# Kernel tuning notes

Hardware: AMD Instinct MI355X
Metric: run time of the kernel (lower is better)

## Reference

```python
import jax, jax.numpy as jnp
import numpy as np

N_RNA, N_PROT, D, C, E = 20000, 5000, 128, 4, 500000

def setup_inputs() -> dict:
    key = jax.random.key(0)
    k1, k2, k3, k4, k5, k6 = jax.random.split(key, 6)
    return {
        "RNA_inputs": jax.random.normal(k1, (N_RNA, D), dtype=jnp.float32),
        "protein_inputs": jax.random.normal(k2, (N_PROT, D), dtype=jnp.float32),
        "RNA_indices": jax.random.randint(k3, (E,), 0, N_RNA, dtype=jnp.int64),
        "protein_indices": jax.random.randint(k4, (E,), 0, N_PROT, dtype=jnp.int64),
        "w_relation": jax.random.normal(k5, (C, D), dtype=jnp.float32),
        "weight_classifier": jax.random.normal(k6, (C, C), dtype=jnp.float32),
    }

def reference(RNA_inputs, protein_inputs, RNA_indices, protein_indices, w_relation, weight_classifier):
    # Gather node features for each pair (dropout p=0.0 -> identity)
    r = RNA_inputs[RNA_indices]        # [E, D]
    p = protein_inputs[protein_indices]  # [E, D]
    # Per-class bilinear: basis[e, c] = sum_d r[e,d] * w_relation[c,d] * p[e,d]
    basis = jnp.einsum('ed,cd->ec', r * p, w_relation)  # [E, C]
    # Classifier matmul + ReLU activation
    return jax.nn.relu(basis @ weight_classifier)  # [E, C]
```

## Files before the change

kernel.cpp:

```cpp
#include <hip/hip_runtime.h>

#define DIM 128
#define NCLS 4

typedef _Float16 f16x4 __attribute__((ext_vector_type(4)));
typedef _Float16 f16x8 __attribute__((ext_vector_type(8)));

__global__ __launch_bounds__(256) void cvt_both_kernel(
    const float* __restrict__ s1, _Float16* __restrict__ d1, int n1,
    const float* __restrict__ s2, _Float16* __restrict__ d2, int n2)
{
    const int total = n1 + n2;
    int i = (blockIdx.x * blockDim.x + threadIdx.x) * 8;
    const int stride = gridDim.x * blockDim.x * 8;
    for (; i < total; i += stride) {
        const float* s; _Float16* d; int j;
        if (i < n1) { s = s1; d = d1; j = i; }
        else        { s = s2; d = d2; j = i - n1; }
        const float4 a = *(const float4*)(s + j);
        const float4 b = *(const float4*)(s + j + 4);
        f16x8 o;
        o[0] = (_Float16)a.x; o[1] = (_Float16)a.y;
        o[2] = (_Float16)a.z; o[3] = (_Float16)a.w;
        o[4] = (_Float16)b.x; o[5] = (_Float16)b.y;
        o[6] = (_Float16)b.z; o[7] = (_Float16)b.w;
        *(f16x8*)(d + j) = o;
    }
}

__device__ __forceinline__ float reduce4(float b0, float b1, float b2, float b3, int lane)
{
    const bool lo1 = (lane & 1) == 0;
    float k0 = lo1 ? b0 : b2, s0 = lo1 ? b2 : b0;
    float k1 = lo1 ? b1 : b3, s1 = lo1 ? b3 : b1;
    float v0 = k0 + __shfl_xor(s0, 1, 32);
    float v1 = k1 + __shfl_xor(s1, 1, 32);
    const bool lo2 = (lane & 2) == 0;
    float k = lo2 ? v0 : v1, s = lo2 ? v1 : v0;
    float v = k + __shfl_xor(s, 2, 32);
    v += __shfl_xor(v, 4, 32);
    v += __shfl_xor(v, 8, 32);
    v += __shfl_xor(v, 16, 32);
    return v;
}

__device__ __forceinline__ void dot_store(
    f16x4 r, f16x4 p, const float4& wf0, const float4& wf1,
    const float4& wf2, const float4& wf3, int lane, int cls,
    float* __restrict__ out, long e)
{
    const f16x4 q = r * p;
    const float qx = (float)q[0], qy = (float)q[1];
    const float qz = (float)q[2], qw = (float)q[3];
    float b0 = qx * wf0.x + qy * wf0.y + qz * wf0.z + qw * wf0.w;
    float b1 = qx * wf1.x + qy * wf1.y + qz * wf1.z + qw * wf1.w;
    float b2 = qx * wf2.x + qy * wf2.y + qz * wf2.z + qw * wf2.w;
    float b3 = qx * wf3.x + qy * wf3.y + qz * wf3.z + qw * wf3.w;
    const float v = reduce4(b0, b1, b2, b3, lane);
    if (lane < 4) out[e * NCLS + cls] = fmaxf(v, 0.0f);
}

__global__ __launch_bounds__(256, 5) void decoder_ilp8_kernel(
    const _Float16* __restrict__ rna,
    const _Float16* __restrict__ prot,
    const int*   __restrict__ ridx,
    const int*   __restrict__ pidx,
    const float* __restrict__ wrel,
    const float* __restrict__ wcls,
    float*       __restrict__ out,
    int nEdges)
{
    const int l32 = threadIdx.x & 31;
    const int hw  = (blockIdx.x * blockDim.x + threadIdx.x) >> 5;
    const int nhw = (gridDim.x * blockDim.x) >> 5;

    const float4 w0 = *(const float4*)(wrel + 0 * DIM + l32 * 4);
    const float4 w1 = *(const float4*)(wrel + 1 * DIM + l32 * 4);
    const float4 w2 = *(const float4*)(wrel + 2 * DIM + l32 * 4);
    const float4 w3 = *(const float4*)(wrel + 3 * DIM + l32 * 4);
    float wc[16];
#pragma unroll
    for (int i = 0; i < 16; ++i) wc[i] = wcls[i];
    float4 wf0, wf1, wf2, wf3;
    {
        float4* wfp[4] = {&wf0, &wf1, &wf2, &wf3};
#pragma unroll
        for (int j = 0; j < 4; ++j) {
            wfp[j]->x = wc[j] * w0.x + wc[4 + j] * w1.x + wc[8 + j] * w2.x + wc[12 + j] * w3.x;
            wfp[j]->y = wc[j] * w0.y + wc[4 + j] * w1.y + wc[8 + j] * w2.y + wc[12 + j] * w3.y;
            wfp[j]->z = wc[j] * w0.z + wc[4 + j] * w1.z + wc[8 + j] * w2.z + wc[12 + j] * w3.z;
            wfp[j]->w = wc[j] * w0.w + wc[4 + j] * w1.w + wc[8 + j] * w2.w + wc[12 + j] * w3.w;
        }
    }
    const int cls = ((l32 & 1) << 1) | ((l32 >> 1) & 1);

    const long step = (long)nhw * 8;
    long e0 = (long)hw * 8;
    if (e0 + 7 >= nEdges) return;

    int4 riA = *(const int4*)(ridx + e0);
    int4 piA = *(const int4*)(pidx + e0);
    int4 riB = *(const int4*)(ridx + e0 + 4);
    int4 piB = *(const int4*)(pidx + e0 + 4);

    for (;;) {
        const f16x4 rA0 = ((const f16x4*)(rna + (size_t)riA.x * DIM))[l32];
        const f16x4 rA1 = ((const f16x4*)(rna + (size_t)riA.y * DIM))[l32];
        const f16x4 rA2 = ((const f16x4*)(rna + (size_t)riA.z * DIM))[l32];
        const f16x4 rA3 = ((const f16x4*)(rna + (size_t)riA.w * DIM))[l32];
        const f16x4 pA0 = ((const f16x4*)(prot + (size_t)piA.x * DIM))[l32];
        const f16x4 pA1 = ((const f16x4*)(prot + (size_t)piA.y * DIM))[l32];
        const f16x4 pA2 = ((const f16x4*)(prot + (size_t)piA.z * DIM))[l32];
        const f16x4 pA3 = ((const f16x4*)(prot + (size_t)piA.w * DIM))[l32];
        const f16x4 rB0 = ((const f16x4*)(rna + (size_t)riB.x * DIM))[l32];
        const f16x4 rB1 = ((const f16x4*)(rna + (size_t)riB.y * DIM))[l32];
        const f16x4 rB2 = ((const f16x4*)(rna + (size_t)riB.z * DIM))[l32];
        const f16x4 rB3 = ((const f16x4*)(rna + (size_t)riB.w * DIM))[l32];
        const f16x4 pB0 = ((const f16x4*)(prot + (size_t)piB.x * DIM))[l32];
        const f16x4 pB1 = ((const f16x4*)(prot + (size_t)piB.y * DIM))[l32];
        const f16x4 pB2 = ((const f16x4*)(prot + (size_t)piB.z * DIM))[l32];
        const f16x4 pB3 = ((const f16x4*)(prot + (size_t)piB.w * DIM))[l32];

        const long en = e0 + step;
        const bool more = (en + 7) < nEdges;
        if (more) {
            riA = *(const int4*)(ridx + en);
            piA = *(const int4*)(pidx + en);
            riB = *(const int4*)(ridx + en + 4);
            piB = *(const int4*)(pidx + en + 4);
        }

        dot_store(rA0, pA0, wf0, wf1, wf2, wf3, l32, cls, out, e0 + 0);
        dot_store(rA1, pA1, wf0, wf1, wf2, wf3, l32, cls, out, e0 + 1);
        dot_store(rA2, pA2, wf0, wf1, wf2, wf3, l32, cls, out, e0 + 2);
        dot_store(rA3, pA3, wf0, wf1, wf2, wf3, l32, cls, out, e0 + 3);
        dot_store(rB0, pB0, wf0, wf1, wf2, wf3, l32, cls, out, e0 + 4);
        dot_store(rB1, pB1, wf0, wf1, wf2, wf3, l32, cls, out, e0 + 5);
        dot_store(rB2, pB2, wf0, wf1, wf2, wf3, l32, cls, out, e0 + 6);
        dot_store(rB3, pB3, wf0, wf1, wf2, wf3, l32, cls, out, e0 + 7);

        if (!more) break;
        e0 = en;
    }
}

__global__ __launch_bounds__(256) void decoder_f32_kernel(
    const float* __restrict__ rna, const float* __restrict__ prot,
    const int* __restrict__ ridx, const int* __restrict__ pidx,
    const float* __restrict__ wrel, const float* __restrict__ wcls,
    float* __restrict__ out, int nEdges)
{
    const int lane32 = threadIdx.x & 31;
    const int hw     = (blockIdx.x * blockDim.x + threadIdx.x) >> 5;
    const int nhw    = (gridDim.x * blockDim.x) >> 5;
    const float4 w0 = *(const float4*)(wrel + 0 * DIM + lane32 * 4);
    const float4 w1 = *(const float4*)(wrel + 1 * DIM + lane32 * 4);
    const float4 w2 = *(const float4*)(wrel + 2 * DIM + lane32 * 4);
    const float4 w3 = *(const float4*)(wrel + 3 * DIM + lane32 * 4);
    float wc[16];
#pragma unroll
    for (int i = 0; i < 16; ++i) wc[i] = wcls[i];
    float4 wf[4];
#pragma unroll
    for (int j = 0; j < 4; ++j) {
        wf[j].x = wc[j] * w0.x + wc[4 + j] * w1.x + wc[8 + j] * w2.x + wc[12 + j] * w3.x;
        wf[j].y = wc[j] * w0.y + wc[4 + j] * w1.y + wc[8 + j] * w2.y + wc[12 + j] * w3.y;
        wf[j].z = wc[j] * w0.z + wc[4 + j] * w1.z + wc[8 + j] * w2.z + wc[12 + j] * w3.z;
        wf[j].w = wc[j] * w0.w + wc[4 + j] * w1.w + wc[8 + j] * w2.w + wc[12 + j] * w3.w;
    }
    const int cls   = ((lane32 & 1) << 1) | ((lane32 >> 1) & 1);
    const int lelem = lane32 * 4;
    for (int e = hw; e < nEdges; e += nhw) {
        const float4 r = *(const float4*)(rna  + (size_t)ridx[e] * DIM + lelem);
        const float4 p = *(const float4*)(prot + (size_t)pidx[e] * DIM + lelem);
        float qx = r.x * p.x, qy = r.y * p.y, qz = r.z * p.z, qw = r.w * p.w;
        float b0 = qx * wf[0].x + qy * wf[0].y + qz * wf[0].z + qw * wf[0].w;
        float b1 = qx * wf[1].x + qy * wf[1].y + qz * wf[1].z + qw * wf[1].w;
        float b2 = qx * wf[2].x + qy * wf[2].y + qz * wf[2].z + qw * wf[2].w;
        float b3 = qx * wf[3].x + qy * wf[3].y + qz * wf[3].z + qw * wf[3].w;
        const float v = reduce4(b0, b1, b2, b3, lane32);
        if (lane32 < 4) out[(size_t)e * NCLS + cls] = fmaxf(v, 0.0f);
    }
}

extern "C" void kernel_launch(void* const* d_in, const int* in_sizes, int n_in,
                              void* d_out, int out_size, void* d_ws, size_t ws_size,
                              hipStream_t stream) {
    const float* rna  = (const float*)d_in[0];
    const float* prot = (const float*)d_in[1];
    const int*   ridx = (const int*)d_in[2];
    const int*   pidx = (const int*)d_in[3];
    const float* wrel = (const float*)d_in[4];
    const float* wcls = (const float*)d_in[5];
    float*       out  = (float*)d_out;

    const int nRnaElems  = in_sizes[0];
    const int nProtElems = in_sizes[1];
    const int nEdges     = in_sizes[2];

    const size_t rnaBytes  = (size_t)nRnaElems * 2;
    const size_t needBytes = rnaBytes + (size_t)nProtElems * 2;

    if (ws_size >= needBytes && (nEdges % 8) == 0 && nEdges >= 8 &&
        (nRnaElems % 8) == 0 && (nProtElems % 8) == 0) {
        _Float16* rnaH  = (_Float16*)d_ws;
        _Float16* protH = (_Float16*)((char*)d_ws + rnaBytes);

        const int totalElems = nRnaElems + nProtElems;
        const int cvtBlocks  = (totalElems / 8 + 255) / 256;
        hipLaunchKernelGGL(cvt_both_kernel, dim3(cvtBlocks), dim3(256), 0, stream,
                           rna, rnaH, nRnaElems, prot, protH, nProtElems);

        hipLaunchKernelGGL(decoder_ilp8_kernel, dim3(2048), dim3(256), 0, stream,
                           rnaH, protH, ridx, pidx, wrel, wcls, out, nEdges);
    } else {
        hipLaunchKernelGGL(decoder_f32_kernel, dim3(8192), dim3(256), 0, stream,
                           rna, prot, ridx, pidx, wrel, wcls, out, nEdges);
    }
}
```

Baseline: 103.7 us.

## Replace shuffle-reduction decoder with MFMA-based edge tile kernel

Replaces the half-wave shuffle-reduction kernel with one where each 64-lane wave handles 32 edges as two 16x16x32 f16 MFMA tiles. The fused weight matrix is built in LDS, cast to f16, and held in registers as the A operand. Each lane now gathers 16-byte row chunks and writes 16-byte output vectors. This removes the cross-lane shuffle reduction and the scalar output stores. In exchange, the fused weights are now rounded to f16, 12 of the 16 MFMA rows are padding, and the fast path now requires the edge count to be a multiple of 32.

```diff
diff --git a/kernel.cpp b/kernel.cpp
--- a/kernel.cpp
+++ b/kernel.cpp
@@ -5,6 +5,7 @@
 
 typedef _Float16 f16x4 __attribute__((ext_vector_type(4)));
 typedef _Float16 f16x8 __attribute__((ext_vector_type(8)));
+typedef float    f32x4 __attribute__((ext_vector_type(4)));
 
 __global__ __launch_bounds__(256) void cvt_both_kernel(
     const float* __restrict__ s1, _Float16* __restrict__ d1, int n1,
@@ -28,7 +29,111 @@
     }
 }
 
-__device__ __forceinline__ float reduce4(float b0, float b1, float b2, float b3, int lane)
+__global__ __launch_bounds__(256, 4) void decoder_mfma_kernel(
+    const _Float16* __restrict__ rna,
+    const _Float16* __restrict__ prot,
+    const int*   __restrict__ ridx,
+    const int*   __restrict__ pidx,
+    const float* __restrict__ wrel,
+    const float* __restrict__ wcls,
+    float*       __restrict__ out,
+    int nEdges)
+{
+    __shared__ _Float16 wf_lds[NCLS][DIM];
+    {
+        const int t = threadIdx.x;
+        if (t < DIM) {
+            const float w0 = wrel[0 * DIM + t];
+            const float w1 = wrel[1 * DIM + t];
+            const float w2 = wrel[2 * DIM + t];
+            const float w3 = wrel[3 * DIM + t];
+#pragma unroll
+            for (int c = 0; c < NCLS; ++c) {
+                wf_lds[c][t] = (_Float16)(w0 * wcls[0 * 4 + c] + w1 * wcls[1 * 4 + c] +
+                                          w2 * wcls[2 * 4 + c] + w3 * wcls[3 * 4 + c]);
+            }
+        }
+    }
+    __syncthreads();
+
+    const int lane = threadIdx.x & 63;
+    const int l16  = lane & 15;
+    const int kg   = lane >> 4;
+
+    f16x8 awf[4];
+    const f16x8 fzero = {};
+#pragma unroll
+    for (int f = 0; f < 4; ++f)
+        awf[f] = (l16 < NCLS) ? *(const f16x8*)(&wf_lds[l16][f * 32 + kg * 8]) : fzero;
+
+    const int wid   = (int)((blockIdx.x * blockDim.x + threadIdx.x) >> 6);
+    const int nw    = (int)((gridDim.x * blockDim.x) >> 6);
+    const int npair = nEdges >> 5;
+
+    const size_t khi  = (size_t)kg * 16;
+    const char* rbase = (const char*)rna  + khi;
+    const char* pbase = (const char*)prot + khi;
+
+    int pr = wid;
+    if (pr >= npair) return;
+
+    int e0  = pr * 32;
+    int riA = ridx[e0 + l16],      piA = pidx[e0 + l16];
+    int riB = ridx[e0 + 16 + l16], piB = pidx[e0 + 16 + l16];
+
+    for (;;) {
+        const char* ra = rbase + ((size_t)riA << 8);
+        const char* pa = pbase + ((size_t)piA << 8);
+        const char* rb = rbase + ((size_t)riB << 8);
+        const char* pb = pbase + ((size_t)piB << 8);
+        f16x8 rAv[4], pAv[4], rBv[4], pBv[4];
+#pragma unroll
+        for (int f = 0; f < 4; ++f) rAv[f] = *(const f16x8*)(ra + f * 64);
+#pragma unroll
+        for (int f = 0; f < 4; ++f) pAv[f] = *(const f16x8*)(pa + f * 64);
+#pragma unroll
+        for (int f = 0; f < 4; ++f) rBv[f] = *(const f16x8*)(rb + f * 64);
+#pragma unroll
+        for (int f = 0; f < 4; ++f) pBv[f] = *(const f16x8*)(pb + f * 64);
+
+        const int  prn  = pr + nw;
+        const bool more = prn < npair;
+        if (more) {
+            const int en = prn * 32;
+            riA = ridx[en + l16];      piA = pidx[en + l16];
+            riB = ridx[en + 16 + l16]; piB = pidx[en + 16 + l16];
+        }
+
+        f32x4 accA = {}, accB = {};
+#pragma unroll
+        for (int f = 0; f < 4; ++f) {
+            const f16x8 q = rAv[f] * pAv[f];
+            accA = __builtin_amdgcn_mfma_f32_16x16x32_f16(awf[f], q, accA, 0, 0, 0);
+        }
+#pragma unroll
+        for (int f = 0; f < 4; ++f) {
+            const f16x8 q = rBv[f] * pBv[f];
+            accB = __builtin_amdgcn_mfma_f32_16x16x32_f16(awf[f], q, accB, 0, 0, 0);
+        }
+
+        if (lane < 16) {
+            f32x4 oA, oB;
+#pragma unroll
+            for (int j = 0; j < 4; ++j) {
+                oA[j] = fmaxf(accA[j], 0.0f);
+                oB[j] = fmaxf(accB[j], 0.0f);
+            }
+            *(f32x4*)(out + (size_t)(e0 + l16) * NCLS)        = oA;
+            *(f32x4*)(out + (size_t)(e0 + 16 + l16) * NCLS)   = oB;
+        }
+
+        if (!more) break;
+        pr = prn;
+        e0 = prn * 32;
+    }
+}
+
+__device__ __forceinline__ float reduce4_f32(float b0, float b1, float b2, float b3, int lane)
 {
     const bool lo1 = (lane & 1) == 0;
     float k0 = lo1 ? b0 : b2, s0 = lo1 ? b2 : b0;
@@ -44,106 +149,6 @@
     return v;
 }
 
-__device__ __forceinline__ void dot_store(
-    f16x4 r, f16x4 p, const float4& wf0, const float4& wf1,
-    const float4& wf2, const float4& wf3, int lane, int cls,
-    float* __restrict__ out, long e)
-{
-    const f16x4 q = r * p;
-    const float qx = (float)q[0], qy = (float)q[1];
-    const float qz = (float)q[2], qw = (float)q[3];
-    float b0 = qx * wf0.x + qy * wf0.y + qz * wf0.z + qw * wf0.w;
-    float b1 = qx * wf1.x + qy * wf1.y + qz * wf1.z + qw * wf1.w;
-    float b2 = qx * wf2.x + qy * wf2.y + qz * wf2.z + qw * wf2.w;
-    float b3 = qx * wf3.x + qy * wf3.y + qz * wf3.z + qw * wf3.w;
-    const float v = reduce4(b0, b1, b2, b3, lane);
-    if (lane < 4) out[e * NCLS + cls] = fmaxf(v, 0.0f);
-}
-
-__global__ __launch_bounds__(256, 5) void decoder_ilp8_kernel(
-    const _Float16* __restrict__ rna,
-    const _Float16* __restrict__ prot,
-    const int*   __restrict__ ridx,
-    const int*   __restrict__ pidx,
-    const float* __restrict__ wrel,
-    const float* __restrict__ wcls,
-    float*       __restrict__ out,
-    int nEdges)
-{
-    const int l32 = threadIdx.x & 31;
-    const int hw  = (blockIdx.x * blockDim.x + threadIdx.x) >> 5;
-    const int nhw = (gridDim.x * blockDim.x) >> 5;
-
-    const float4 w0 = *(const float4*)(wrel + 0 * DIM + l32 * 4);
-    const float4 w1 = *(const float4*)(wrel + 1 * DIM + l32 * 4);
-    const float4 w2 = *(const float4*)(wrel + 2 * DIM + l32 * 4);
-    const float4 w3 = *(const float4*)(wrel + 3 * DIM + l32 * 4);
-    float wc[16];
-#pragma unroll
-    for (int i = 0; i < 16; ++i) wc[i] = wcls[i];
-    float4 wf0, wf1, wf2, wf3;
-    {
-        float4* wfp[4] = {&wf0, &wf1, &wf2, &wf3};
-#pragma unroll
-        for (int j = 0; j < 4; ++j) {
-            wfp[j]->x = wc[j] * w0.x + wc[4 + j] * w1.x + wc[8 + j] * w2.x + wc[12 + j] * w3.x;
-            wfp[j]->y = wc[j] * w0.y + wc[4 + j] * w1.y + wc[8 + j] * w2.y + wc[12 + j] * w3.y;
-            wfp[j]->z = wc[j] * w0.z + wc[4 + j] * w1.z + wc[8 + j] * w2.z + wc[12 + j] * w3.z;
-            wfp[j]->w = wc[j] * w0.w + wc[4 + j] * w1.w + wc[8 + j] * w2.w + wc[12 + j] * w3.w;
-        }
-    }
-    const int cls = ((l32 & 1) << 1) | ((l32 >> 1) & 1);
-
-    const long step = (long)nhw * 8;
-    long e0 = (long)hw * 8;
-    if (e0 + 7 >= nEdges) return;
-
-    int4 riA = *(const int4*)(ridx + e0);
-    int4 piA = *(const int4*)(pidx + e0);
-    int4 riB = *(const int4*)(ridx + e0 + 4);
-    int4 piB = *(const int4*)(pidx + e0 + 4);
-
-    for (;;) {
-        const f16x4 rA0 = ((const f16x4*)(rna + (size_t)riA.x * DIM))[l32];
-        const f16x4 rA1 = ((const f16x4*)(rna + (size_t)riA.y * DIM))[l32];
-        const f16x4 rA2 = ((const f16x4*)(rna + (size_t)riA.z * DIM))[l32];
-        const f16x4 rA3 = ((const f16x4*)(rna + (size_t)riA.w * DIM))[l32];
-        const f16x4 pA0 = ((const f16x4*)(prot + (size_t)piA.x * DIM))[l32];
-        const f16x4 pA1 = ((const f16x4*)(prot + (size_t)piA.y * DIM))[l32];
-        const f16x4 pA2 = ((const f16x4*)(prot + (size_t)piA.z * DIM))[l32];
-        const f16x4 pA3 = ((const f16x4*)(prot + (size_t)piA.w * DIM))[l32];
-        const f16x4 rB0 = ((const f16x4*)(rna + (size_t)riB.x * DIM))[l32];
-        const f16x4 rB1 = ((const f16x4*)(rna + (size_t)riB.y * DIM))[l32];
-        const f16x4 rB2 = ((const f16x4*)(rna + (size_t)riB.z * DIM))[l32];
-        const f16x4 rB3 = ((const f16x4*)(rna + (size_t)riB.w * DIM))[l32];
-        const f16x4 pB0 = ((const f16x4*)(prot + (size_t)piB.x * DIM))[l32];
-        const f16x4 pB1 = ((const f16x4*)(prot + (size_t)piB.y * DIM))[l32];
-        const f16x4 pB2 = ((const f16x4*)(prot + (size_t)piB.z * DIM))[l32];
-        const f16x4 pB3 = ((const f16x4*)(prot + (size_t)piB.w * DIM))[l32];
-
-        const long en = e0 + step;
-        const bool more = (en + 7) < nEdges;
-        if (more) {
-            riA = *(const int4*)(ridx + en);
-            piA = *(const int4*)(pidx + en);
-            riB = *(const int4*)(ridx + en + 4);
-            piB = *(const int4*)(pidx + en + 4);
-        }
-
-        dot_store(rA0, pA0, wf0, wf1, wf2, wf3, l32, cls, out, e0 + 0);
-        dot_store(rA1, pA1, wf0, wf1, wf2, wf3, l32, cls, out, e0 + 1);
-        dot_store(rA2, pA2, wf0, wf1, wf2, wf3, l32, cls, out, e0 + 2);
-        dot_store(rA3, pA3, wf0, wf1, wf2, wf3, l32, cls, out, e0 + 3);
-        dot_store(rB0, pB0, wf0, wf1, wf2, wf3, l32, cls, out, e0 + 4);
-        dot_store(rB1, pB1, wf0, wf1, wf2, wf3, l32, cls, out, e0 + 5);
-        dot_store(rB2, pB2, wf0, wf1, wf2, wf3, l32, cls, out, e0 + 6);
-        dot_store(rB3, pB3, wf0, wf1, wf2, wf3, l32, cls, out, e0 + 7);
-
-        if (!more) break;
-        e0 = en;
-    }
-}
-
 __global__ __launch_bounds__(256) void decoder_f32_kernel(
     const float* __restrict__ rna, const float* __restrict__ prot,
     const int* __restrict__ ridx, const int* __restrict__ pidx,
@@ -178,7 +183,7 @@
         float b1 = qx * wf[1].x + qy * wf[1].y + qz * wf[1].z + qw * wf[1].w;
         float b2 = qx * wf[2].x + qy * wf[2].y + qz * wf[2].z + qw * wf[2].w;
         float b3 = qx * wf[3].x + qy * wf[3].y + qz * wf[3].z + qw * wf[3].w;
-        const float v = reduce4(b0, b1, b2, b3, lane32);
+        const float v = reduce4_f32(b0, b1, b2, b3, lane32);
         if (lane32 < 4) out[(size_t)e * NCLS + cls] = fmaxf(v, 0.0f);
     }
 }
@@ -201,7 +206,7 @@
     const size_t rnaBytes  = (size_t)nRnaElems * 2;
     const size_t needBytes = rnaBytes + (size_t)nProtElems * 2;
 
-    if (ws_size >= needBytes && (nEdges % 8) == 0 && nEdges >= 8 &&
+    if (ws_size >= needBytes && (nEdges % 32) == 0 && nEdges >= 32 &&
         (nRnaElems % 8) == 0 && (nProtElems % 8) == 0) {
         _Float16* rnaH  = (_Float16*)d_ws;
         _Float16* protH = (_Float16*)((char*)d_ws + rnaBytes);
@@ -211,7 +216,7 @@
         hipLaunchKernelGGL(cvt_both_kernel, dim3(cvtBlocks), dim3(256), 0, stream,
                            rna, rnaH, nRnaElems, prot, protH, nProtElems);
 
-        hipLaunchKernelGGL(decoder_ilp8_kernel, dim3(2048), dim3(256), 0, stream,
+        hipLaunchKernelGGL(decoder_mfma_kernel, dim3(1024), dim3(256), 0, stream,
                            rnaH, protH, ridx, pidx, wrel, wcls, out, nEdges);
     } else {
         hipLaunchKernelGGL(decoder_f32_kernel, dim3(8192), dim3(256), 0, stream,
```

After: 106.1 us. 2.4% more time.
